# Optimization experiments

Measured on AMD Instinct MI355X. Metric: run time of the kernel, lower is better.

Reference implementation:

```python
import jax, jax.numpy as jnp
import numpy as np

WS = 8          # window_size
HEADS = 8
HEAD_DIM = 32
DIM = 256       # input_dim
DISP = WS // 2  # displacement for shifted windows
SCALE = HEAD_DIM ** -0.5
NEG = float('-inf')


def _create_mask(upper_lower, left_right):
    S = WS * WS
    m = np.zeros((S, S), np.float32)
    if upper_lower:
        m[-DISP * WS:, :-DISP * WS] = NEG
        m[:-DISP * WS, -DISP * WS:] = NEG
    if left_right:
        m = m.reshape(WS, WS, WS, WS)
        m[:, -DISP:, :, :-DISP] = NEG
        m[:, :-DISP, :, -DISP:] = NEG
        m = m.reshape(S, S)
    return m


def _shift_mask(nwh, nww):
    # per-window additive mask, [nW, S, S]
    S = WS * WS
    low = _create_mask(True, False)
    right = _create_mask(False, True)
    mask = np.zeros((nwh * nww, S, S), np.float32)
    mask[-nww:] += low                 # bottom row of windows
    mask[nww - 1::nww] += right        # rightmost column of windows
    return mask


def _rel_idx():
    coords = np.array([[x, y] for x in range(WS) for y in range(WS)])
    dist = coords[None, :, :] - coords[:, None, :] + (WS - 1)  # in [0, 2*WS-2]
    return dist[..., 0], dist[..., 1]


def setup_inputs() -> dict:
    key = jax.random.key(0)
    ks = jax.random.split(key, 5)
    B, H, W = 64, 64, 64
    inner = HEADS * HEAD_DIM
    return {
        "x": jax.random.normal(ks[0], (B, H, W, DIM), jnp.float32),
        "qkv_w": jax.random.normal(ks[1], (3 * inner, DIM), jnp.float32) * 0.02,
        "proj_w": jax.random.normal(ks[2], (DIM, inner), jnp.float32) * 0.02,
        "proj_b": jnp.zeros((DIM,), jnp.float32),
        "pos_emb": jax.random.normal(ks[3], (2 * WS - 1, 2 * WS - 1), jnp.float32),
    }


def reference(x, qkv_w, proj_w, proj_b, pos_emb):
    B, H, W, C = x.shape
    nwh, nww = H // WS, W // WS
    nW, S = nwh * nww, WS * WS

    x = jnp.roll(x, (-DISP, -DISP), axis=(1, 2))          # cyclic shift
    qkv = x @ qkv_w.T                                      # [B,H,W,3*inner]
    q, k, v = jnp.split(qkv, 3, axis=-1)

    def towin(t):  # [B,H,W,heads*d] -> [B,heads,nW,S,d]
        t = t.reshape(B, nwh, WS, nww, WS, HEADS, HEAD_DIM)
        return t.transpose(0, 5, 1, 3, 2, 4, 6).reshape(B, HEADS, nW, S, HEAD_DIM)

    q, k, v = towin(q), towin(k), towin(v)

    scores = jnp.einsum('bhwid,bhwjd->bhwij', q, k) * SCALE
    ri, ci = _rel_idx()
    scores = scores + pos_emb[ri, ci]                      # relative position bias [S,S]
    mask = jnp.asarray(_shift_mask(nwh, nww))              # [nW,S,S]
    scores = scores + mask[None, None]

    attn = jax.nn.softmax(scores, axis=-1)
    out = jnp.einsum('bhwij,bhwjd->bhwid', attn, v)        # [B,heads,nW,S,d]

    out = out.reshape(B, HEADS, nwh, nww, WS, WS, HEAD_DIM)
    out = out.transpose(0, 2, 4, 3, 5, 1, 6).reshape(B, H, W, HEADS * HEAD_DIM)

    out = out @ proj_w.T + proj_b
    out = jnp.roll(out, (DISP, DISP), axis=(1, 2))         # reverse cyclic shift
    return out
```

## Files before the change

### kernel.cpp

```cpp
#include <hip/hip_runtime.h>
#include <hip/hip_bf16.h>
#include <math.h>

typedef __bf16 bf16;
typedef bf16 bf16x8 __attribute__((ext_vector_type(8)));
typedef bf16 bf16x4 __attribute__((ext_vector_type(4)));
typedef float f32x4 __attribute__((ext_vector_type(4)));

#define MFMA16(A,B,C) __builtin_amdgcn_mfma_f32_16x16x32_bf16(A,B,C,0,0,0)

static constexpr int QKV_ELEMS  = 768 * 256;
static constexpr int PROJ_ELEMS = 256 * 256;
static constexpr size_t QKVWS_ELEMS = (size_t)4096 * 8 * 6144;

static __device__ __forceinline__ unsigned pack2(float a, float b) {
    bf16 xa = (bf16)a, xb = (bf16)b;
    unsigned short ua, ub;
    __builtin_memcpy(&ua, &xa, 2);
    __builtin_memcpy(&ub, &xb, 2);
    return (unsigned)ua | ((unsigned)ub << 16);
}

#define BUILD_FRAG(dst, PKL0, PKL1, PKH0, PKH1)                               \
  {                                                                            \
    int sA = ((lane & 16) << 1) + lo;                                          \
    int sB = sA + 16;                                                          \
    int a0 = __shfl((int)(PKL0), sA), a1 = __shfl((int)(PKL1), sA);            \
    int a2 = __shfl((int)(PKL0), sB), a3 = __shfl((int)(PKL1), sB);            \
    int b0 = __shfl((int)(PKH0), sA), b1 = __shfl((int)(PKH1), sA);            \
    int b2 = __shfl((int)(PKH0), sB), b3 = __shfl((int)(PKH1), sB);            \
    union { int w[4]; bf16x8 v; } u_;                                          \
    bool uh_ = (lane >= 32);                                                   \
    u_.w[0] = uh_ ? b0 : a0; u_.w[1] = uh_ ? b1 : a1;                          \
    u_.w[2] = uh_ ? b2 : a2; u_.w[3] = uh_ ? b3 : a3;                          \
    dst = u_.v;                                                                \
  }

__global__ void cvt_weights(const float* __restrict__ qkv_w,
                            const float* __restrict__ proj_w,
                            bf16* __restrict__ wq, bf16* __restrict__ wp) {
    int i = blockIdx.x * 256 + threadIdx.x;
    if (i < QKV_ELEMS) wq[i] = (bf16)qkv_w[i];
    int j = i - QKV_ELEMS;
    if (j >= 0 && j < PROJ_ELEMS) wp[j] = (bf16)proj_w[j];
}

__global__ __launch_bounds__(256, 2)
void swin_qkv(const float* __restrict__ x,
              const bf16* __restrict__ wqkv,
              bf16* __restrict__ qkv_ws)
{
    __shared__ alignas(16) unsigned char xbuf[64 * 512];

    const int tid  = threadIdx.x;
    const int wave = tid >> 6, lane = tid & 63;
    const int hi   = lane >> 4, lo = lane & 15;
    const int b    = blockIdx.x >> 6;
    const int w    = blockIdx.x & 63;
    const int wh   = w >> 3, wwi = w & 7;
    const f32x4 zero4 = {0.f, 0.f, 0.f, 0.f};

    {
        int tok = tid >> 2, j = tid & 3;
        int gy = ((wh << 3) + (tok >> 3) + 4) & 63;
        int gx = ((wwi << 3) + (tok & 7) + 4) & 63;
        const float* src = x + (((b << 6) + gy) * 64 + gx) * 256;
        #pragma unroll
        for (int f = 0; f < 16; ++f) {
            int c4 = f * 4 + j;
            float4 v = *(const float4*)(src + c4 * 4);
            bf16x4 bv;
            bv[0] = (bf16)v.x; bv[1] = (bf16)v.y; bv[2] = (bf16)v.z; bv[3] = (bf16)v.w;
            int chunk = (c4 >> 1) ^ (tok & 7);
            *(bf16x4*)(xbuf + tok * 512 + (chunk << 4) + ((c4 & 1) << 3)) = bv;
        }
    }
    __syncthreads();

    bf16* base0 = qkv_ws + ((size_t)blockIdx.x * 8 + 2 * wave) * 6144;

    #pragma unroll
    for (int pass = 0; pass < 3; ++pass) {
        const int secb = pass * 256 + 64 * wave;

        bf16x8 af[8][4];
        #pragma unroll
        for (int kk = 0; kk < 8; ++kk)
            #pragma unroll
            for (int Mt = 0; Mt < 4; ++Mt)
                af[kk][Mt] = *(const bf16x8*)(wqkv + (secb + 16 * Mt + lo) * 256 + kk * 32 + hi * 8);

        f32x4 acc[4][4];
        #pragma unroll
        for (int Mt = 0; Mt < 4; ++Mt)
            #pragma unroll
            for (int Nt = 0; Nt < 4; ++Nt) acc[Mt][Nt] = zero4;
        #pragma unroll
        for (int kk = 0; kk < 8; ++kk) {
            bf16x8 bx[4];
            #pragma unroll
            for (int Nt = 0; Nt < 4; ++Nt) {
                int tok = Nt * 16 + lo;
                bx[Nt] = *(const bf16x8*)(xbuf + tok * 512 + (((kk * 4 + hi) ^ (tok & 7)) << 4));
            }
            #pragma unroll
            for (int Mt = 0; Mt < 4; ++Mt)
                #pragma unroll
                for (int Nt = 0; Nt < 4; ++Nt)
                    acc[Mt][Nt] = MFMA16(af[kk][Mt], bx[Nt], acc[Mt][Nt]);
        }

        if (pass < 2) {
            #pragma unroll
            for (int Mt = 0; Mt < 4; ++Mt) {
                bf16* hb = base0 + (Mt >> 1) * 6144 + pass * 2048;
                int d0 = ((Mt & 1) << 4) + 4 * hi;
                #pragma unroll
                for (int Nt = 0; Nt < 4; ++Nt) {
                    int tok = Nt * 16 + lo;
                    bf16x4 v;
                    #pragma unroll
                    for (int r = 0; r < 4; ++r) v[r] = (bf16)acc[Mt][Nt][r];
                    *(bf16x4*)(hb + tok * 32 + d0) = v;
                }
            }
        } else {
            #pragma unroll
            for (int Mt = 0; Mt < 4; ++Mt) {
                bf16* hb = base0 + (Mt >> 1) * 6144 + 4096;
                #pragma unroll
                for (int Nt = 0; Nt < 4; ++Nt) {
                    int tok = Nt * 16 + lo;
                    #pragma unroll
                    for (int r = 0; r < 4; ++r) {
                        int d = ((Mt & 1) << 4) + 4 * hi + r;
                        hb[d * 64 + tok] = (bf16)acc[Mt][Nt][r];
                    }
                }
            }
        }
    }
}

__global__ __launch_bounds__(256, 2)
void swin_attn_proj(const bf16* __restrict__ qkv_ws,
                    const bf16* __restrict__ wproj,
                    const float* __restrict__ proj_b,
                    const float* __restrict__ pose_g,
                    float* __restrict__ out)
{
    __shared__ alignas(16) unsigned char xbuf[64 * 512];
    __shared__ float pose[225];

    const int tid  = threadIdx.x;
    const int wave = tid >> 6, lane = tid & 63;
    const int hi   = lane >> 4, lo = lane & 15;
    const int b    = blockIdx.x >> 6;
    const int w    = blockIdx.x & 63;
    const int wh   = w >> 3, wwi = w & 7;
    const bool mlow = (wh == 7), mright = (wwi == 7);
    const f32x4 zero4 = {0.f, 0.f, 0.f, 0.f};

    if (tid < 225) pose[tid] = pose_g[tid];
    __syncthreads();

    const bool colmask_ = mright && (((lo & 7) >= 4) != (hi & 1));

    bf16x8 fr[2][12];
    {
        const bf16* b0 = qkv_ws + ((size_t)blockIdx.x * 8 + 2 * wave) * 6144;
        #pragma unroll
        for (int hp = 0; hp < 2; ++hp) {
            const bf16* bb = b0 + hp * 6144;
            #pragma unroll
            for (int i = 0; i < 4; ++i) {
                fr[hp][i]     = *(const bf16x8*)(bb + 2048 + (16 * i + lo) * 32 + hi * 8);
                fr[hp][4 + i] = *(const bf16x8*)(bb + (16 * i + lo) * 32 + hi * 8);
                fr[hp][8 + i] = *(const bf16x8*)(bb + 4096 + (16 * (i & 1) + lo) * 64 + (i >> 1) * 32 + hi * 8);
            }
        }
    }

    #pragma unroll
    for (int hp = 0; hp < 2; ++hp) {
        const int h = 2 * wave + hp;

        #pragma unroll
        for (int it = 0; it < 4; ++it) {
            f32x4 s4[4];
            #pragma unroll
            for (int jt = 0; jt < 4; ++jt) s4[jt] = MFMA16(fr[hp][jt], fr[hp][4 + it], zero4);

            float mx = -INFINITY;
            #pragma unroll
            for (int jt = 0; jt < 4; ++jt) {
                bool tilemask = mlow && ((it >= 2) != (jt >= 2));
                #pragma unroll
                for (int r = 0; r < 4; ++r) {
                    int drow = 2 * jt + (hi >> 1) - 2 * it - (lo >> 3) + 7;
                    int dcol = 4 * (hi & 1) + r - (lo & 7) + 7;
                    float s = s4[jt][r] * 0.17677669529663687f + pose[drow * 15 + dcol];
                    if (tilemask | colmask_) s = -INFINITY;
                    s4[jt][r] = s;
                    mx = fmaxf(mx, s);
                }
            }
            mx = fmaxf(mx, __shfl_xor(mx, 16));
            mx = fmaxf(mx, __shfl_xor(mx, 32));
            float sum = 0.f;
            #pragma unroll
            for (int jt = 0; jt < 4; ++jt)
                #pragma unroll
                for (int r = 0; r < 4; ++r) {
                    float e = __expf(s4[jt][r] - mx);
                    s4[jt][r] = e; sum += e;
                }
            sum += __shfl_xor(sum, 16);
            sum += __shfl_xor(sum, 32);
            float riv = 1.0f / sum;

            unsigned pk[4][2];
            #pragma unroll
            for (int jt = 0; jt < 4; ++jt)
                #pragma unroll
                for (int p = 0; p < 2; ++p)
                    pk[jt][p] = pack2(s4[jt][2 * p], s4[jt][2 * p + 1]);

            f32x4 o2[2] = {zero4, zero4};
            #pragma unroll
            for (int ks = 0; ks < 2; ++ks) {
                bf16x8 pB;
                BUILD_FRAG(pB, pk[2 * ks][0], pk[2 * ks][1], pk[2 * ks + 1][0], pk[2 * ks + 1][1]);
                #pragma unroll
                for (int dMt = 0; dMt < 2; ++dMt)
                    o2[dMt] = MFMA16(fr[hp][8 + ks * 2 + dMt], pB, o2[dMt]);
            }
            #pragma unroll
            for (int dMt = 0; dMt < 2; ++dMt) {
                int tok = it * 16 + lo;
                bf16x4 v;
                #pragma unroll
                for (int r = 0; r < 4; ++r) v[r] = (bf16)(o2[dMt][r] * riv);
                int chunk = ((h << 2) + (dMt << 1) + (hi >> 1)) ^ (tok & 7);
                *(bf16x4*)(xbuf + tok * 512 + (chunk << 4) + ((hi & 1) << 3)) = v;
            }
        }
    }
    __syncthreads();

    bf16x8 bB[8][4];
    #pragma unroll
    for (int kk = 0; kk < 8; ++kk)
        #pragma unroll
        for (int nt = 0; nt < 4; ++nt) {
            int c = wave * 64 + nt * 16 + lo;
            bB[kk][nt] = *(const bf16x8*)(wproj + c * 256 + kk * 32 + hi * 8);
        }

    f32x4 pacc[4][4];
    #pragma unroll
    for (int Mt = 0; Mt < 4; ++Mt)
        #pragma unroll
        for (int nt = 0; nt < 4; ++nt) pacc[Mt][nt] = zero4;
    #pragma unroll
    for (int kk = 0; kk < 8; ++kk) {
        bf16x8 aA[4];
        #pragma unroll
        for (int Mt = 0; Mt < 4; ++Mt) {
            int tok = Mt * 16 + lo;
            aA[Mt] = *(const bf16x8*)(xbuf + tok * 512 + (((kk * 4 + hi) ^ (tok & 7)) << 4));
        }
        #pragma unroll
        for (int Mt = 0; Mt < 4; ++Mt)
            #pragma unroll
            for (int nt = 0; nt < 4; ++nt)
                pacc[Mt][nt] = MFMA16(aA[Mt], bB[kk][nt], pacc[Mt][nt]);
    }
    #pragma unroll
    for (int nt = 0; nt < 4; ++nt) {
        int c = wave * 64 + nt * 16 + lo;
        float pb2 = proj_b[c];
        #pragma unroll
        for (int Mt = 0; Mt < 4; ++Mt)
            #pragma unroll
            for (int r = 0; r < 4; ++r) {
                int tok = Mt * 16 + 4 * hi + r;
                int fy = ((wh << 3) + (tok >> 3) + 4) & 63;
                int fx = ((wwi << 3) + (tok & 7) + 4) & 63;
                out[(((b << 6) + fy) * 64 + fx) * 256 + c] = pacc[Mt][nt][r] + pb2;
            }
    }
}

extern "C" void kernel_launch(void* const* d_in, const int* in_sizes, int n_in,
                              void* d_out, int out_size, void* d_ws, size_t ws_size,
                              hipStream_t stream) {
    const float* x       = (const float*)d_in[0];
    const float* qkv_w   = (const float*)d_in[1];
    const float* proj_w  = (const float*)d_in[2];
    const float* proj_b  = (const float*)d_in[3];
    const float* pos_emb = (const float*)d_in[4];

    bf16* wq = (bf16*)d_ws;
    bf16* wp = wq + QKV_ELEMS;
    bf16* qkv_ws = wp + PROJ_ELEMS;

    cvt_weights<<<dim3((QKV_ELEMS + PROJ_ELEMS) / 256), dim3(256), 0, stream>>>(
        qkv_w, proj_w, wq, wp);
    swin_qkv<<<dim3(64 * 64), dim3(256), 0, stream>>>(x, wq, qkv_ws);
    swin_attn_proj<<<dim3(64 * 64), dim3(256), 0, stream>>>(
        qkv_ws, wp, proj_b, pos_emb, (float*)d_out);
}
```

Before: 489.5 us.

## Load x tile via global_load_lds and stage V transpose through LDS

The x tile is now copied straight from global memory into LDS as fp32 using global_load_lds, without passing through registers, and is converted to bf16 when the MFMA B-fragments are read. This doubles the LDS footprint for the tile. The V output, which is stored transposed, is first written into a per-wave swizzled LDS buffer and then written to global memory as 16-byte vector stores instead of scattered 2-byte stores. The cost is more shared memory, which may lower occupancy, plus extra conversion work in the inner loop.

```diff
diff --git a/kernel.cpp b/kernel.cpp
--- a/kernel.cpp
+++ b/kernel.cpp
@@ -12,6 +12,11 @@
 static constexpr int QKV_ELEMS  = 768 * 256;
 static constexpr int PROJ_ELEMS = 256 * 256;
 static constexpr size_t QKVWS_ELEMS = (size_t)4096 * 8 * 6144;
+
+static __device__ __forceinline__ void lds_fence() {
+    asm volatile("s_waitcnt lgkmcnt(0)" ::: "memory");
+    __builtin_amdgcn_sched_barrier(0);
+}
 
 static __device__ __forceinline__ unsigned pack2(float a, float b) {
     bf16 xa = (bf16)a, xb = (bf16)b;
@@ -50,7 +55,8 @@
               const bf16* __restrict__ wqkv,
               bf16* __restrict__ qkv_ws)
 {
-    __shared__ alignas(16) unsigned char xbuf[64 * 512];
+    __shared__ alignas(16) unsigned char xbuf[64 * 1024];
+    __shared__ alignas(16) unsigned char vtbuf[4][4096];
 
     const int tid  = threadIdx.x;
     const int wave = tid >> 6, lane = tid & 63;
@@ -60,22 +66,29 @@
     const int wh   = w >> 3, wwi = w & 7;
     const f32x4 zero4 = {0.f, 0.f, 0.f, 0.f};
 
-    {
-        int tok = tid >> 2, j = tid & 3;
+    #pragma unroll
+    for (int i = 0; i < 16; ++i) {
+        int tok = wave * 16 + i;
         int gy = ((wh << 3) + (tok >> 3) + 4) & 63;
         int gx = ((wwi << 3) + (tok & 7) + 4) & 63;
-        const float* src = x + (((b << 6) + gy) * 64 + gx) * 256;
-        #pragma unroll
-        for (int f = 0; f < 16; ++f) {
-            int c4 = f * 4 + j;
-            float4 v = *(const float4*)(src + c4 * 4);
-            bf16x4 bv;
-            bv[0] = (bf16)v.x; bv[1] = (bf16)v.y; bv[2] = (bf16)v.z; bv[3] = (bf16)v.w;
-            int chunk = (c4 >> 1) ^ (tok & 7);
-            *(bf16x4*)(xbuf + tok * 512 + (chunk << 4) + ((c4 & 1) << 3)) = bv;
-        }
-    }
+        const float* srow = x + (((b << 6) + gy) * 64 + gx) * 256;
+        const float* src  = srow + ((lane ^ (tok & 7)) << 2);
+        __builtin_amdgcn_global_load_lds(
+            (const __attribute__((address_space(1))) unsigned int*)src,
+            (__attribute__((address_space(3))) unsigned int*)(xbuf + tok * 1024),
+            16, 0, 0);
+    }
+    asm volatile("s_waitcnt vmcnt(0)" ::: "memory");
     __syncthreads();
+
+    auto ldx = [&](int tok, int c16 ) -> bf16x8 {
+        const float4 a = *(const float4*)(xbuf + tok * 1024 + ((c16 ^ (tok & 7)) << 4));
+        const float4 c = *(const float4*)(xbuf + tok * 1024 + (((c16 + 1) ^ (tok & 7)) << 4));
+        union { unsigned u[4]; bf16x8 v; } r;
+        r.u[0] = pack2(a.x, a.y); r.u[1] = pack2(a.z, a.w);
+        r.u[2] = pack2(c.x, c.y); r.u[3] = pack2(c.z, c.w);
+        return r.v;
+    };
 
     bf16* base0 = qkv_ws + ((size_t)blockIdx.x * 8 + 2 * wave) * 6144;
 
@@ -99,10 +112,8 @@
         for (int kk = 0; kk < 8; ++kk) {
             bf16x8 bx[4];
             #pragma unroll
-            for (int Nt = 0; Nt < 4; ++Nt) {
-                int tok = Nt * 16 + lo;
-                bx[Nt] = *(const bf16x8*)(xbuf + tok * 512 + (((kk * 4 + hi) ^ (tok & 7)) << 4));
-            }
+            for (int Nt = 0; Nt < 4; ++Nt)
+                bx[Nt] = ldx(Nt * 16 + lo, 8 * kk + 2 * hi);
             #pragma unroll
             for (int Mt = 0; Mt < 4; ++Mt)
                 #pragma unroll
@@ -125,18 +136,34 @@
                 }
             }
         } else {
-            #pragma unroll
-            for (int Mt = 0; Mt < 4; ++Mt) {
-                bf16* hb = base0 + (Mt >> 1) * 6144 + 4096;
-                #pragma unroll
-                for (int Nt = 0; Nt < 4; ++Nt) {
-                    int tok = Nt * 16 + lo;
+            unsigned char* vt = vtbuf[wave];
+            #pragma unroll
+            for (int hh = 0; hh < 2; ++hh) {
+                #pragma unroll
+                for (int m = 0; m < 2; ++m) {
+                    int Mt = 2 * hh + m;
                     #pragma unroll
-                    for (int r = 0; r < 4; ++r) {
-                        int d = ((Mt & 1) << 4) + 4 * hi + r;
-                        hb[d * 64 + tok] = (bf16)acc[Mt][Nt][r];
+                    for (int Nt = 0; Nt < 4; ++Nt) {
+                        int tok = Nt * 16 + lo;
+                        #pragma unroll
+                        for (int r = 0; r < 4; ++r) {
+                            int d = (m << 4) + 4 * hi + r;
+                            int byte = d * 128 + ((2 * tok) ^ (hi << 5));
+                            *(bf16*)(vt + byte) = (bf16)acc[Mt][Nt][r];
+                        }
                     }
                 }
+                lds_fence();
+                bf16* hb = base0 + hh * 6144 + 4096;
+                #pragma unroll
+                for (int i = 0; i < 4; ++i) {
+                    int d    = lane >> 1;
+                    int tok0 = ((lane & 1) << 3) + (i << 4);
+                    int byte = d * 128 + ((2 * tok0) ^ (((d >> 2) & 3) << 5));
+                    bf16x8 vv = *(const bf16x8*)(vt + byte);
+                    *(bf16x8*)(hb + d * 64 + tok0) = vv;
+                }
+                lds_fence();
             }
         }
     }
```

Result: faster. 446.5 us (-8.8%).
